# Performance work log

Measured on AMD Instinct MI355X. Metric: run time of the kernel, lower is better.

Reference implementation:

```python
import jax, jax.numpy as jnp
import numpy as np

GRID_SIZE = 5
SPLINE_ORDER = 3
GRID_RANGE = (-1.0, 1.0)
LAYERS = [1024, 1024, 1024]
BATCH = 8192
LN_EPS = 1e-5


def _make_grid(in_features):
    h = (GRID_RANGE[1] - GRID_RANGE[0]) / GRID_SIZE
    n = GRID_SIZE + 2 * SPLINE_ORDER + 1  # 12 knots
    g = jnp.linspace(GRID_RANGE[0] - h * SPLINE_ORDER,
                     GRID_RANGE[1] + h * SPLINE_ORDER, n, dtype=jnp.float32)
    return jnp.broadcast_to(g, (in_features, n))


def setup_inputs() -> dict:
    key = jax.random.key(0)
    ks = jax.random.split(key, 8)
    n_layers = len(LAYERS) - 1
    d_in, d_out = LAYERS[0], LAYERS[1]  # square layers -> stackable params
    coeff = GRID_SIZE + SPLINE_ORDER  # 8
    # kaiming_uniform_(nonlinearity='linear'): bound = sqrt(3) * (1/sqrt(fan_in))
    bw_bound = float(np.sqrt(3.0) / np.sqrt(d_in))
    sw_bound = float(np.sqrt(3.0) / np.sqrt(d_in * coeff))
    x = jax.random.normal(ks[0], (BATCH, d_in), dtype=jnp.float32)
    base_w = jax.random.uniform(ks[1], (n_layers, d_out, d_in), jnp.float32, -bw_bound, bw_bound)
    spline_w = jax.random.uniform(ks[2], (n_layers, d_out, d_in, coeff), jnp.float32, -sw_bound, sw_bound)
    ln_g = jnp.ones((n_layers, d_out), jnp.float32)
    ln_b = jnp.zeros((n_layers, d_out), jnp.float32)
    prelu_a = jnp.full((n_layers,), 0.25, jnp.float32)
    grid = jnp.stack([_make_grid(d_in) for _ in range(n_layers)])  # [L, in, 12]
    return {"x": x, "base_w": base_w, "spline_w": spline_w,
            "ln_g": ln_g, "ln_b": ln_b, "prelu_a": prelu_a, "grid": grid}


def _bspline_bases(x, g):
    """Cox-de Boor recursion. x: [B, in], g: [in, n_knots] -> [B, in, G+order]."""
    xu = x[..., None]  # [B, in, 1]
    bases = ((xu >= g[:, :-1]) & (xu < g[:, 1:])).astype(x.dtype)  # [B, in, 11]
    for k in range(1, SPLINE_ORDER + 1):
        left = g[:, :-(k + 1)]
        right = g[:, k:-1]
        delta = jnp.where(right == left, jnp.ones_like(right), right - left)
        bases = ((xu - left) / delta * bases[..., :-1]
                 + (g[:, k + 1:] - xu) / (g[:, k + 1:] - g[:, 1:-k]) * bases[..., 1:])
    return bases  # [B, in, 8]


def kan_forward(x, base_w, spline_w, ln_g, ln_b, prelu_a, grid):
    n_layers = base_w.shape[0]
    for i in range(n_layers):
        base_out = jnp.matmul(jax.nn.gelu(x, approximate=False), base_w[i].T)  # [B, out]
        bases = _bspline_bases(x, grid[i])  # [B, in, 8]
        spline_out = jnp.matmul(bases.reshape(x.shape[0], -1),
                                spline_w[i].reshape(spline_w.shape[1], -1).T)  # [B, out]
        h = base_out + spline_out
        mu = jnp.mean(h, axis=-1, keepdims=True)
        var = jnp.var(h, axis=-1, keepdims=True)  # biased, matches torch LayerNorm
        h = (h - mu) * jax.lax.rsqrt(var + LN_EPS) * ln_g[i] + ln_b[i]
        x = jnp.where(h >= 0, h, prelu_a[i] * h)  # PReLU (scalar slope per layer)
    return x


def reference(x, base_w, spline_w, ln_g, ln_b, prelu_a, grid):
    return kan_forward(x, base_w, spline_w, ln_g, ln_b, prelu_a, grid)
```

## Files before the change

### kernel.cpp

```cpp
#include <hip/hip_runtime.h>
#include <hip/hip_bf16.h>
#include <cstdint>
#include <cstddef>

typedef __bf16 bf16_t;
typedef __bf16 bf16x8 __attribute__((ext_vector_type(8)));
typedef __bf16 bf16x4 __attribute__((ext_vector_type(4)));
typedef float  f32x4  __attribute__((ext_vector_type(4)));

#define DIM    1024
#define NCOEF  8
#define KTOT   (DIM + DIM * NCOEF)
#define NKNOT  12
#define BATCH  8192
#define LN_EPS 1e-5f

__device__ __forceinline__ float gelu_exact(float x) {
    return 0.5f * x * (1.0f + erff(x * 0.70710678118654752440f));
}

__device__ __forceinline__ void gl_lds16(const void* g, void* l) {
    __builtin_amdgcn_global_load_lds(
        (const __attribute__((address_space(1))) unsigned int*)(uintptr_t)g,
        (__attribute__((address_space(3))) unsigned int*)(uintptr_t)l, 16, 0, 0);
}

__device__ __forceinline__ uint64_t pack4bf(float a, float b, float c, float d) {
    union { bf16_t h[4]; uint64_t q; } u;
    u.h[0] = (bf16_t)a; u.h[1] = (bf16_t)b; u.h[2] = (bf16_t)c; u.h[3] = (bf16_t)d;
    return u.q;
}

__device__ __forceinline__ void spline8(float x, float g0, float invh,
                                        uint64_t& lo, uint64_t& hi) {
    float u = (x - g0) * invh;
    float jf = floorf(u);
    int j = (int)jf;
    float f = u - jf;
    float f2 = f * f, f3 = f2 * f;
    float om = 1.0f - f, om2 = om * om;
    float w0 = om2 * om * (1.0f / 6.0f);
    float w3 = f3 * (1.0f / 6.0f);
    float w1 = fmaf(0.5f, f3, 2.0f / 3.0f) - f2;
    float w2 = 1.0f - w0 - w1 - w3;
    uint64_t W64 = pack4bf(w0, w1, w2, w3);
    if (!(u >= 0.0f && u < 11.0f)) W64 = 0;
    int sh = (j - 3) * 16;
    if (sh >= 0) {
        int s = sh & 63;
        uint64_t loW = W64 << s;
        uint64_t hiW = s ? (W64 >> (64 - s)) : 0ull;
        lo = (sh < 64) ? loW : 0ull;
        hi = (sh < 64) ? hiW : loW;
    } else {
        lo = W64 >> (-sh);
        hi = 0ull;
    }
}

__global__ void pack_w(const float* __restrict__ bw, const float* __restrict__ sw,
                       bf16_t* __restrict__ W) {
    int idx = blockIdx.x * 256 + threadIdx.x;
    bf16_t* wrow = W + (size_t)(idx >> 10) * KTOT;
    int j = idx & 1023;
    wrow[j] = (bf16_t)bw[idx];
    const float4* sp = (const float4*)(sw + (size_t)idx * NCOEF);
    float4 s0 = sp[0], s1 = sp[1];
    bf16x8 v;
    v[0] = (bf16_t)s0.x; v[1] = (bf16_t)s0.y; v[2] = (bf16_t)s0.z; v[3] = (bf16_t)s0.w;
    v[4] = (bf16_t)s1.x; v[5] = (bf16_t)s1.y; v[6] = (bf16_t)s1.z; v[7] = (bf16_t)s1.w;
    *(bf16x8*)(wrow + DIM + j * NCOEF) = v;
}

__global__ void prep_A(const float* __restrict__ x, bf16_t* __restrict__ A,
                       const float* __restrict__ gp) {
    const int row = blockIdx.x, t = threadIdx.x;
    const float g0 = gp[0];
    const float invh = 1.0f / (gp[1] - gp[0]);
    f32x4 v = *(const f32x4*)(x + (size_t)row * DIM + t * 4);
    bf16_t* Ar = A + (size_t)row * KTOT;
    bf16x4 ge;
#pragma unroll
    for (int k = 0; k < 4; k++) ge[k] = (bf16_t)gelu_exact(v[k]);
    *(bf16x4*)(Ar + t * 4) = ge;
#pragma unroll
    for (int k = 0; k < 4; k++) {
        uint64_t lo, hi;
        union { uint64_t u[2]; uint4 q; } o;
        spline8(v[k], g0, invh, lo, hi);
        o.u[0] = lo; o.u[1] = hi;
        *(uint4*)(Ar + DIM + (t * 4 + k) * NCOEF) = o.q;
    }
}


#define STR2(x) #x
#define GATEV(N) asm volatile("s_waitcnt vmcnt(" STR2(N) ")" ::: "memory");
#define LGKM(N)  asm volatile("s_waitcnt lgkmcnt(" STR2(N) ")" ::: "memory");
#define BAR() { __builtin_amdgcn_s_barrier(); asm volatile("" ::: "memory"); }

#define MF_ROW(I, A_) \
    acc[I][0] = __builtin_amdgcn_mfma_f32_16x16x32_bf16(A_, b0, acc[I][0], 0, 0, 0); \
    acc[I][1] = __builtin_amdgcn_mfma_f32_16x16x32_bf16(A_, b1, acc[I][1], 0, 0, 0); \
    acc[I][2] = __builtin_amdgcn_mfma_f32_16x16x32_bf16(A_, b2, acc[I][2], 0, 0, 0); \
    acc[I][3] = __builtin_amdgcn_mfma_f32_16x16x32_bf16(A_, b3, acc[I][3], 0, 0, 0);

#define TILE(T, S, SN, SP, DOSTAGE, GATESTMT, DOEARLY, WAITB) { \
     \
    if (DOSTAGE) { \
      gl_lds16(Ag0 + (size_t)((T) + 3) * 32, ldsA + (SP) * 8192 + tid * 8); \
      gl_lds16(Ag1 + (size_t)((T) + 3) * 32, ldsA + (SP) * 8192 + 4096 + tid * 8); } \
    BAR() \
    { const bf16_t* Ab_ = ldsA + (S) * 8192 + aOff; \
      a4 = *(const bf16x8*)(Ab_ + 2048); a5 = *(const bf16x8*)(Ab_ + 2560); \
      a6 = *(const bf16x8*)(Ab_ + 3072); a7 = *(const bf16x8*)(Ab_ + 3584); } \
    LGKM(4) \
    __builtin_amdgcn_sched_barrier(0); \
    __builtin_amdgcn_s_setprio(1); \
    MF_ROW(0, a0) MF_ROW(1, a1) MF_ROW(2, a2) MF_ROW(3, a3) \
    __builtin_amdgcn_s_setprio(0); \
    BAR() \
     \
    if (DOSTAGE) { \
      gl_lds16(Bg0 + (size_t)((T) + 3) * 32, ldsB + (SP) * 8192 + tid * 8); \
      gl_lds16(Bg1 + (size_t)((T) + 3) * 32, ldsB + (SP) * 8192 + 4096 + tid * 8); } \
    GATESTMT \
    BAR() \
    if (DOEARLY) { \
      const bf16_t* An_ = ldsA + (SN) * 8192 + aOff; \
      const bf16_t* Bn_ = ldsB + (SN) * 8192 + bOff; \
      na0 = *(const bf16x8*)(An_);        na1 = *(const bf16x8*)(An_ + 512); \
      na2 = *(const bf16x8*)(An_ + 1024); na3 = *(const bf16x8*)(An_ + 1536); \
      nb0 = *(const bf16x8*)(Bn_);        nb1 = *(const bf16x8*)(Bn_ + 512); \
      nb2 = *(const bf16x8*)(Bn_ + 1024); nb3 = *(const bf16x8*)(Bn_ + 1536); } \
    WAITB \
    __builtin_amdgcn_sched_barrier(0); \
    __builtin_amdgcn_s_setprio(1); \
    MF_ROW(4, a4) MF_ROW(5, a5) MF_ROW(6, a6) MF_ROW(7, a7) \
    __builtin_amdgcn_s_setprio(0); \
    BAR() \
    a0 = na0; a1 = na1; a2 = na2; a3 = na3; \
    b0 = nb0; b1 = nb1; b2 = nb2; b3 = nb3; \
}

#define PSTAGE(T, S) \
    gl_lds16(Ag0 + (size_t)(T) * 32, ldsA + (S) * 8192 + tid * 8); \
    gl_lds16(Ag1 + (size_t)(T) * 32, ldsA + (S) * 8192 + 4096 + tid * 8); \
    gl_lds16(Bg0 + (size_t)(T) * 32, ldsB + (S) * 8192 + tid * 8); \
    gl_lds16(Bg1 + (size_t)(T) * 32, ldsB + (S) * 8192 + 4096 + tid * 8);

template<int NTK>
__global__ __launch_bounds__(512, 2) void gemm_ab(
    const bf16_t* __restrict__ A,
    const bf16_t* __restrict__ W,
    float* __restrict__ C,
    int mmask, int mshift, int rows) {
    __shared__ __align__(16) bf16_t lds[65536];
    bf16_t* __restrict__ ldsA = lds;
    bf16_t* __restrict__ ldsB = lds + 32768;

    const int tid = threadIdx.x;
    const int l = tid & 63, wv = tid >> 6;
    const int wm = wv >> 2, wn = wv & 3;

    const int chunk = gridDim.x >> 3;
    const int bid = blockIdx.x;
    const int wg = (bid & 7) * chunk + (bid >> 3);
    const int bm = wg & mmask;
    const int bn = (wg >> mshift) & 3;
    const int ks = wg >> (mshift + 2);
    const int row0 = bm << 8, col0 = bn << 8;
    const int koff0 = ks * (NTK * 32);

    const int srow = tid >> 2;
    const int slc = (tid & 3) ^ ((srow >> 1) & 3);
    const bf16_t* __restrict__ Ag0 = A + (size_t)(row0 + srow) * KTOT + koff0 + slc * 8;
    const bf16_t* __restrict__ Ag1 = Ag0 + (size_t)128 * KTOT;
    const bf16_t* __restrict__ Bg0 = W + (size_t)(col0 + srow) * KTOT + koff0 + slc * 8;
    const bf16_t* __restrict__ Bg1 = Bg0 + (size_t)128 * KTOT;

    const int l15 = l & 15;
    const int pc = (l >> 4) ^ ((l15 >> 1) & 3);
    const int aOff = (wm * 128 + l15) * 32 + pc * 8;
    const int bOff = (wn * 64 + l15) * 32 + pc * 8;

    f32x4 acc[8][4] = {};
    bf16x8 a0, a1, a2, a3, a4, a5, a6, a7, b0, b1, b2, b3;
    bf16x8 na0, na1, na2, na3, nb0, nb1, nb2, nb3;

    PSTAGE(0, 0)
    PSTAGE(1, 1)
    PSTAGE(2, 2)
    GATEV(8)
    BAR()
    {
        const bf16_t* An_ = ldsA + aOff;
        const bf16_t* Bn_ = ldsB + bOff;
        a0 = *(const bf16x8*)(An_);        a1 = *(const bf16x8*)(An_ + 512);
        a2 = *(const bf16x8*)(An_ + 1024); a3 = *(const bf16x8*)(An_ + 1536);
        b0 = *(const bf16x8*)(Bn_);        b1 = *(const bf16x8*)(Bn_ + 512);
        b2 = *(const bf16x8*)(Bn_ + 1024); b3 = *(const bf16x8*)(Bn_ + 1536);
    }

#pragma unroll 1
    for (int t = 0; t < NTK - 4; t += 4) {
        TILE(t + 0, 0, 1, 3, 1, GATEV(8), 1, LGKM(8))
        TILE(t + 1, 1, 2, 0, 1, GATEV(8), 1, LGKM(8))
        TILE(t + 2, 2, 3, 1, 1, GATEV(8), 1, LGKM(8))
        TILE(t + 3, 3, 0, 2, 1, GATEV(8), 1, LGKM(8))
    }
    TILE(NTK - 4, 0, 1, 3, 1, GATEV(8), 1, LGKM(8))
    TILE(NTK - 3, 1, 2, 0, 0, GATEV(4), 1, LGKM(8))
    TILE(NTK - 2, 2, 3, 1, 0, GATEV(0), 1, LGKM(8))
    TILE(NTK - 1, 3, 0, 2, 0, ;,        0, LGKM(0))

    float* __restrict__ Cp = C + (size_t)ks * rows * DIM;
    const int r0 = row0 + wm * 128 + (l >> 4) * 4;
    const int c0 = col0 + wn * 64 + l15;
#pragma unroll
    for (int i = 0; i < 8; i++)
#pragma unroll
        for (int j = 0; j < 4; j++)
#pragma unroll
            for (int r = 0; r < 4; r++)
                Cp[(size_t)(r0 + i * 16 + r) * DIM + c0 + j * 16] = acc[i][j][r];
}

__global__ void ln_mid_A(const float* __restrict__ h, int rows, int ksplit,
                         const float* __restrict__ g_ln, const float* __restrict__ b_ln,
                         const float* __restrict__ pa, bf16_t* __restrict__ A,
                         const float* __restrict__ gp) {
    const int row = blockIdx.x, tid = threadIdx.x;
    const int w = tid >> 6, l = tid & 63;
    f32x4 v = {0.0f, 0.0f, 0.0f, 0.0f};
    for (int ks = 0; ks < ksplit; ks++)
        v += *(const f32x4*)(h + ((size_t)ks * rows + row) * DIM + tid * 4);
    float s = v[0] + v[1] + v[2] + v[3];
    float q = v[0] * v[0] + v[1] * v[1] + v[2] * v[2] + v[3] * v[3];
#pragma unroll
    for (int o = 32; o > 0; o >>= 1) { s += __shfl_xor(s, o); q += __shfl_xor(q, o); }
    __shared__ float rs[4], rq[4];
    if (l == 0) { rs[w] = s; rq[w] = q; }
    __syncthreads();
    s = rs[0] + rs[1] + rs[2] + rs[3];
    q = rq[0] + rq[1] + rq[2] + rq[3];
    float mean = s * (1.0f / DIM);
    float var = q * (1.0f / DIM) - mean * mean;
    float rstd = rsqrtf(var + LN_EPS);
    float a = pa[0];
    const float g0 = gp[0];
    const float invh = 1.0f / (gp[1] - gp[0]);
    bf16_t* Ar = A + (size_t)row * KTOT;
    bf16x4 ge;
#pragma unroll
    for (int c = 0; c < 4; c++) {
        int col = tid * 4 + c;
        float yv = (v[c] - mean) * rstd * g_ln[col] + b_ln[col];
        yv = (yv >= 0.0f) ? yv : a * yv;
        ge[c] = (bf16_t)gelu_exact(yv);
        uint64_t lo, hi;
        union { uint64_t u[2]; uint4 qv; } o;
        spline8(yv, g0, invh, lo, hi);
        o.u[0] = lo; o.u[1] = hi;
        *(uint4*)(Ar + DIM + (size_t)col * NCOEF) = o.qv;
    }
    *(bf16x4*)(Ar + tid * 4) = ge;
}

__global__ void ln_out(const float* __restrict__ h, int rows, int ksplit,
                       const float* __restrict__ g_ln, const float* __restrict__ b_ln,
                       const float* __restrict__ pa, float* __restrict__ out) {
    const int row = blockIdx.x, tid = threadIdx.x;
    const int w = tid >> 6, l = tid & 63;
    f32x4 v = {0.0f, 0.0f, 0.0f, 0.0f};
    for (int ks = 0; ks < ksplit; ks++)
        v += *(const f32x4*)(h + ((size_t)ks * rows + row) * DIM + tid * 4);
    float s = v[0] + v[1] + v[2] + v[3];
    float q = v[0] * v[0] + v[1] * v[1] + v[2] * v[2] + v[3] * v[3];
#pragma unroll
    for (int o = 32; o > 0; o >>= 1) { s += __shfl_xor(s, o); q += __shfl_xor(q, o); }
    __shared__ float rs[4], rq[4];
    if (l == 0) { rs[w] = s; rq[w] = q; }
    __syncthreads();
    s = rs[0] + rs[1] + rs[2] + rs[3];
    q = rq[0] + rq[1] + rq[2] + rq[3];
    float mean = s * (1.0f / DIM);
    float var = q * (1.0f / DIM) - mean * mean;
    float rstd = rsqrtf(var + LN_EPS);
    float a = pa[0];
    f32x4 o4;
#pragma unroll
    for (int c = 0; c < 4; c++) {
        int col = tid * 4 + c;
        float yv = (v[c] - mean) * rstd * g_ln[col] + b_ln[col];
        o4[c] = (yv >= 0.0f) ? yv : a * yv;
    }
    *(f32x4*)(out + (size_t)row * DIM + tid * 4) = o4;
}

extern "C" void kernel_launch(void* const* d_in, const int* in_sizes, int n_in,
                              void* d_out, int out_size, void* d_ws, size_t ws_size,
                              hipStream_t stream) {
    const float* x    = (const float*)d_in[0];
    const float* bw   = (const float*)d_in[1];
    const float* sw   = (const float*)d_in[2];
    const float* ln_g = (const float*)d_in[3];
    const float* ln_b = (const float*)d_in[4];
    const float* pa   = (const float*)d_in[5];
    const float* gridK = (const float*)d_in[6];
    float* out = (float*)d_out;

    const size_t wbytes = (size_t)2 * DIM * KTOT * sizeof(bf16_t);
    int R = 8192, ksplit = 2;
    for (;;) {
        size_t need = wbytes + (size_t)R * KTOT * 2 + (size_t)ksplit * R * DIM * 4;
        if (need <= ws_size || R == 512) break;
        R >>= 1;
        int mt = R / 256;
        ksplit = (mt >= 32) ? 2 : (mt >= 16) ? 4 : 8;
    }
    int mtiles = R / 256;
    int mshift = 0; while ((1 << mshift) < mtiles) mshift++;
    int mmask = mtiles - 1;
    int grid = mtiles * 4 * ksplit;

    char* wsc = (char*)d_ws;
    bf16_t* Wbuf = (bf16_t*)wsc;
    bf16_t* Abuf = (bf16_t*)(wsc + wbytes);
    float*  hbuf = (float*)(wsc + wbytes + (size_t)R * KTOT * 2);

    pack_w<<<(2 * DIM * DIM) / 256, 256, 0, stream>>>(bw, sw, Wbuf);

    auto launch_gemm = [&](const bf16_t* Wl, hipStream_t st) {
        if (ksplit == 2)
            gemm_ab<144><<<grid, 512, 0, st>>>(Abuf, Wl, hbuf, mmask, mshift, R);
        else if (ksplit == 4)
            gemm_ab<72><<<grid, 512, 0, st>>>(Abuf, Wl, hbuf, mmask, mshift, R);
        else
            gemm_ab<36><<<grid, 512, 0, st>>>(Abuf, Wl, hbuf, mmask, mshift, R);
    };

    const int nslab = BATCH / R;
    for (int sidx = 0; sidx < nslab; sidx++) {
        const size_t row0 = (size_t)sidx * R;
        const float* x0 = x + row0 * DIM;
        prep_A<<<R, 256, 0, stream>>>(x0, Abuf, gridK);
        launch_gemm(Wbuf, stream);
        ln_mid_A<<<R, 256, 0, stream>>>(hbuf, R, ksplit, ln_g, ln_b, pa,
                                        Abuf, gridK + DIM * NKNOT);
        launch_gemm(Wbuf + (size_t)DIM * KTOT, stream);
        ln_out<<<R, 256, 0, stream>>>(hbuf, R, ksplit, ln_g + DIM, ln_b + DIM,
                                      pa + 1, out + row0 * DIM);
    }
}
```

Before: 568.2 us.

## Double-buffer GEMM fragment registers to drop barriers; grid-stride elementwise kernels

The GEMM main loop now alternates between two named register sets (even/odd) for A/B fragments instead of copying next-tile fragments into current registers. This removes the register copies and two of the four block barriers per K-tile, leaving one barrier before the early LDS reads and one at tile end. The prep, mid-layernorm and output-layernorm kernels become grid-stride loops over a capped grid of 2048 blocks, which cuts block launch overhead. Fewer barriers could expose LDS write-after-read hazards across the 4-stage ring, and the extra fragment registers raise VGPR pressure under the 2-waves-per-SIMD launch bound.

```diff
diff --git a/kernel.cpp b/kernel.cpp
--- a/kernel.cpp
+++ b/kernel.cpp
@@ -73,23 +73,25 @@
 }
 
 __global__ void prep_A(const float* __restrict__ x, bf16_t* __restrict__ A,
-                       const float* __restrict__ gp) {
-    const int row = blockIdx.x, t = threadIdx.x;
+                       const float* __restrict__ gp, int R) {
+    const int t = threadIdx.x;
     const float g0 = gp[0];
     const float invh = 1.0f / (gp[1] - gp[0]);
-    f32x4 v = *(const f32x4*)(x + (size_t)row * DIM + t * 4);
-    bf16_t* Ar = A + (size_t)row * KTOT;
-    bf16x4 ge;
-#pragma unroll
-    for (int k = 0; k < 4; k++) ge[k] = (bf16_t)gelu_exact(v[k]);
-    *(bf16x4*)(Ar + t * 4) = ge;
-#pragma unroll
-    for (int k = 0; k < 4; k++) {
-        uint64_t lo, hi;
-        union { uint64_t u[2]; uint4 q; } o;
-        spline8(v[k], g0, invh, lo, hi);
-        o.u[0] = lo; o.u[1] = hi;
-        *(uint4*)(Ar + DIM + (t * 4 + k) * NCOEF) = o.q;
+    for (int row = blockIdx.x; row < R; row += gridDim.x) {
+        f32x4 v = *(const f32x4*)(x + (size_t)row * DIM + t * 4);
+        bf16_t* Ar = A + (size_t)row * KTOT;
+        bf16x4 ge;
+#pragma unroll
+        for (int k = 0; k < 4; k++) ge[k] = (bf16_t)gelu_exact(v[k]);
+        *(bf16x4*)(Ar + t * 4) = ge;
+#pragma unroll
+        for (int k = 0; k < 4; k++) {
+            uint64_t lo, hi;
+            union { uint64_t u[2]; uint4 q; } o;
+            spline8(v[k], g0, invh, lo, hi);
+            o.u[0] = lo; o.u[1] = hi;
+            *(uint4*)(Ar + DIM + (t * 4 + k) * NCOEF) = o.q;
+        }
     }
 }
 
@@ -99,48 +101,51 @@
 #define LGKM(N)  asm volatile("s_waitcnt lgkmcnt(" STR2(N) ")" ::: "memory");
 #define BAR() { __builtin_amdgcn_s_barrier(); asm volatile("" ::: "memory"); }
 
-#define MF_ROW(I, A_) \
-    acc[I][0] = __builtin_amdgcn_mfma_f32_16x16x32_bf16(A_, b0, acc[I][0], 0, 0, 0); \
-    acc[I][1] = __builtin_amdgcn_mfma_f32_16x16x32_bf16(A_, b1, acc[I][1], 0, 0, 0); \
-    acc[I][2] = __builtin_amdgcn_mfma_f32_16x16x32_bf16(A_, b2, acc[I][2], 0, 0, 0); \
-    acc[I][3] = __builtin_amdgcn_mfma_f32_16x16x32_bf16(A_, b3, acc[I][3], 0, 0, 0);
-
-#define TILE(T, S, SN, SP, DOSTAGE, GATESTMT, DOEARLY, WAITB) { \
+#define EA(i) ea##i
+#define EB(i) eb##i
+#define OA(i) oa##i
+#define OB(i) ob##i
+
+#define MF_ROWX(I, A_, CB) \
+    acc[I][0] = __builtin_amdgcn_mfma_f32_16x16x32_bf16(A_, CB(0), acc[I][0], 0, 0, 0); \
+    acc[I][1] = __builtin_amdgcn_mfma_f32_16x16x32_bf16(A_, CB(1), acc[I][1], 0, 0, 0); \
+    acc[I][2] = __builtin_amdgcn_mfma_f32_16x16x32_bf16(A_, CB(2), acc[I][2], 0, 0, 0); \
+    acc[I][3] = __builtin_amdgcn_mfma_f32_16x16x32_bf16(A_, CB(3), acc[I][3], 0, 0, 0);
+
+#define TILE(T, S, SN, SP, STG, GATESTMT, RD, WAITB, CA, CB, NA, NB) { \
      \
-    if (DOSTAGE) { \
+    if (STG) { \
       gl_lds16(Ag0 + (size_t)((T) + 3) * 32, ldsA + (SP) * 8192 + tid * 8); \
       gl_lds16(Ag1 + (size_t)((T) + 3) * 32, ldsA + (SP) * 8192 + 4096 + tid * 8); } \
-    BAR() \
     { const bf16_t* Ab_ = ldsA + (S) * 8192 + aOff; \
-      a4 = *(const bf16x8*)(Ab_ + 2048); a5 = *(const bf16x8*)(Ab_ + 2560); \
-      a6 = *(const bf16x8*)(Ab_ + 3072); a7 = *(const bf16x8*)(Ab_ + 3584); } \
+      CA(4) = *(const bf16x8*)(Ab_ + 2048); CA(5) = *(const bf16x8*)(Ab_ + 2560); \
+      CA(6) = *(const bf16x8*)(Ab_ + 3072); CA(7) = *(const bf16x8*)(Ab_ + 3584); } \
     LGKM(4) \
     __builtin_amdgcn_sched_barrier(0); \
     __builtin_amdgcn_s_setprio(1); \
-    MF_ROW(0, a0) MF_ROW(1, a1) MF_ROW(2, a2) MF_ROW(3, a3) \
+    MF_ROWX(0, CA(0), CB) MF_ROWX(1, CA(1), CB) \
+    MF_ROWX(2, CA(2), CB) MF_ROWX(3, CA(3), CB) \
     __builtin_amdgcn_s_setprio(0); \
-    BAR() \
      \
-    if (DOSTAGE) { \
+    if (STG) { \
       gl_lds16(Bg0 + (size_t)((T) + 3) * 32, ldsB + (SP) * 8192 + tid * 8); \
       gl_lds16(Bg1 + (size_t)((T) + 3) * 32, ldsB + (SP) * 8192 + 4096 + tid * 8); } \
     GATESTMT \
-    BAR() \
-    if (DOEARLY) { \
+    if (RD) { \
+      BAR() \
       const bf16_t* An_ = ldsA + (SN) * 8192 + aOff; \
       const bf16_t* Bn_ = ldsB + (SN) * 8192 + bOff; \
-      na0 = *(const bf16x8*)(An_);        na1 = *(const bf16x8*)(An_ + 512); \
-      na2 = *(const bf16x8*)(An_ + 1024); na3 = *(const bf16x8*)(An_ + 1536); \
-      nb0 = *(const bf16x8*)(Bn_);        nb1 = *(const bf16x8*)(Bn_ + 512); \
-      nb2 = *(const bf16x8*)(Bn_ + 1024); nb3 = *(const bf16x8*)(Bn_ + 1536); } \
+      NA(0) = *(const bf16x8*)(An_);        NA(1) = *(const bf16x8*)(An_ + 512); \
+      NA(2) = *(const bf16x8*)(An_ + 1024); NA(3) = *(const bf16x8*)(An_ + 1536); \
+      NB(0) = *(const bf16x8*)(Bn_);        NB(1) = *(const bf16x8*)(Bn_ + 512); \
+      NB(2) = *(const bf16x8*)(Bn_ + 1024); NB(3) = *(const bf16x8*)(Bn_ + 1536); } \
     WAITB \
     __builtin_amdgcn_sched_barrier(0); \
     __builtin_amdgcn_s_setprio(1); \
-    MF_ROW(4, a4) MF_ROW(5, a5) MF_ROW(6, a6) MF_ROW(7, a7) \
+    MF_ROWX(4, CA(4), CB) MF_ROWX(5, CA(5), CB) \
+    MF_ROWX(6, CA(6), CB) MF_ROWX(7, CA(7), CB) \
     __builtin_amdgcn_s_setprio(0); \
     BAR() \
-    a0 = na0; a1 = na1; a2 = na2; a3 = na3; \
-    b0 = nb0; b1 = nb1; b2 = nb2; b3 = nb3; \
 }
 
 #define PSTAGE(T, S) \
@@ -185,8 +190,8 @@
     const int bOff = (wn * 64 + l15) * 32 + pc * 8;
 
     f32x4 acc[8][4] = {};
-    bf16x8 a0, a1, a2, a3, a4, a5, a6, a7, b0, b1, b2, b3;
-    bf16x8 na0, na1, na2, na3, nb0, nb1, nb2, nb3;
+    bf16x8 ea0, ea1, ea2, ea3, ea4, ea5, ea6, ea7, eb0, eb1, eb2, eb3;
+    bf16x8 oa0, oa1, oa2, oa3, oa4, oa5, oa6, oa7, ob0, ob1, ob2, ob3;
 
     PSTAGE(0, 0)
     PSTAGE(1, 1)
@@ -196,23 +201,23 @@
     {
         const bf16_t* An_ = ldsA + aOff;
         const bf16_t* Bn_ = ldsB + bOff;
-        a0 = *(const bf16x8*)(An_);        a1 = *(const bf16x8*)(An_ + 512);
-        a2 = *(const bf16x8*)(An_ + 1024); a3 = *(const bf16x8*)(An_ + 1536);
-        b0 = *(const bf16x8*)(Bn_);        b1 = *(const bf16x8*)(Bn_ + 512);
-        b2 = *(const bf16x8*)(Bn_ + 1024); b3 = *(const bf16x8*)(Bn_ + 1536);
+        ea0 = *(const bf16x8*)(An_);        ea1 = *(const bf16x8*)(An_ + 512);
+        ea2 = *(const bf16x8*)(An_ + 1024); ea3 = *(const bf16x8*)(An_ + 1536);
+        eb0 = *(const bf16x8*)(Bn_);        eb1 = *(const bf16x8*)(Bn_ + 512);
+        eb2 = *(const bf16x8*)(Bn_ + 1024); eb3 = *(const bf16x8*)(Bn_ + 1536);
     }
 
 #pragma unroll 1
     for (int t = 0; t < NTK - 4; t += 4) {
-        TILE(t + 0, 0, 1, 3, 1, GATEV(8), 1, LGKM(8))
-        TILE(t + 1, 1, 2, 0, 1, GATEV(8), 1, LGKM(8))
-        TILE(t + 2, 2, 3, 1, 1, GATEV(8), 1, LGKM(8))
-        TILE(t + 3, 3, 0, 2, 1, GATEV(8), 1, LGKM(8))
-    }
-    TILE(NTK - 4, 0, 1, 3, 1, GATEV(8), 1, LGKM(8))
-    TILE(NTK - 3, 1, 2, 0, 0, GATEV(4), 1, LGKM(8))
-    TILE(NTK - 2, 2, 3, 1, 0, GATEV(0), 1, LGKM(8))
-    TILE(NTK - 1, 3, 0, 2, 0, ;,        0, LGKM(0))
+        TILE(t + 0, 0, 1, 3, 1, GATEV(8), 1, LGKM(8), EA, EB, OA, OB)
+        TILE(t + 1, 1, 2, 0, 1, GATEV(8), 1, LGKM(8), OA, OB, EA, EB)
+        TILE(t + 2, 2, 3, 1, 1, GATEV(8), 1, LGKM(8), EA, EB, OA, OB)
+        TILE(t + 3, 3, 0, 2, 1, GATEV(8), 1, LGKM(8), OA, OB, EA, EB)
+    }
+    TILE(NTK - 4, 0, 1, 3, 1, GATEV(8), 1, LGKM(8), EA, EB, OA, OB)
+    TILE(NTK - 3, 1, 2, 0, 0, GATEV(4), 1, LGKM(8), OA, OB, EA, EB)
+    TILE(NTK - 2, 2, 3, 1, 0, GATEV(0), 1, LGKM(8), EA, EB, OA, OB)
+    TILE(NTK - 1, 3, 0, 2, 0, GATEV(0), 0, LGKM(0), OA, OB, EA, EB)
 
     float* __restrict__ Cp = C + (size_t)ks * rows * DIM;
     const int r0 = row0 + wm * 128 + (l >> 4) * 4;
@@ -230,72 +235,78 @@
                          const float* __restrict__ g_ln, const float* __restrict__ b_ln,
                          const float* __restrict__ pa, bf16_t* __restrict__ A,
                          const float* __restrict__ gp) {
-    const int row = blockIdx.x, tid = threadIdx.x;
+    const int tid = threadIdx.x;
     const int w = tid >> 6, l = tid & 63;
-    f32x4 v = {0.0f, 0.0f, 0.0f, 0.0f};
-    for (int ks = 0; ks < ksplit; ks++)
-        v += *(const f32x4*)(h + ((size_t)ks * rows + row) * DIM + tid * 4);
-    float s = v[0] + v[1] + v[2] + v[3];
-    float q = v[0] * v[0] + v[1] * v[1] + v[2] * v[2] + v[3] * v[3];
-#pragma unroll
-    for (int o = 32; o > 0; o >>= 1) { s += __shfl_xor(s, o); q += __shfl_xor(q, o); }
-    __shared__ float rs[4], rq[4];
-    if (l == 0) { rs[w] = s; rq[w] = q; }
-    __syncthreads();
-    s = rs[0] + rs[1] + rs[2] + rs[3];
-    q = rq[0] + rq[1] + rq[2] + rq[3];
-    float mean = s * (1.0f / DIM);
-    float var = q * (1.0f / DIM) - mean * mean;
-    float rstd = rsqrtf(var + LN_EPS);
-    float a = pa[0];
+    const float a = pa[0];
     const float g0 = gp[0];
     const float invh = 1.0f / (gp[1] - gp[0]);
-    bf16_t* Ar = A + (size_t)row * KTOT;
-    bf16x4 ge;
-#pragma unroll
-    for (int c = 0; c < 4; c++) {
-        int col = tid * 4 + c;
-        float yv = (v[c] - mean) * rstd * g_ln[col] + b_ln[col];
-        yv = (yv >= 0.0f) ? yv : a * yv;
-        ge[c] = (bf16_t)gelu_exact(yv);
-        uint64_t lo, hi;
-        union { uint64_t u[2]; uint4 qv; } o;
-        spline8(yv, g0, invh, lo, hi);
-        o.u[0] = lo; o.u[1] = hi;
-        *(uint4*)(Ar + DIM + (size_t)col * NCOEF) = o.qv;
-    }
-    *(bf16x4*)(Ar + tid * 4) = ge;
+    __shared__ float rs[4], rq[4];
+    for (int row = blockIdx.x; row < rows; row += gridDim.x) {
+        f32x4 v = {0.0f, 0.0f, 0.0f, 0.0f};
+        for (int ks = 0; ks < ksplit; ks++)
+            v += *(const f32x4*)(h + ((size_t)ks * rows + row) * DIM + tid * 4);
+        float s = v[0] + v[1] + v[2] + v[3];
+        float q = v[0] * v[0] + v[1] * v[1] + v[2] * v[2] + v[3] * v[3];
+#pragma unroll
+        for (int o = 32; o > 0; o >>= 1) { s += __shfl_xor(s, o); q += __shfl_xor(q, o); }
+        if (l == 0) { rs[w] = s; rq[w] = q; }
+        __syncthreads();
+        s = rs[0] + rs[1] + rs[2] + rs[3];
+        q = rq[0] + rq[1] + rq[2] + rq[3];
+        __syncthreads();
+        float mean = s * (1.0f / DIM);
+        float var = q * (1.0f / DIM) - mean * mean;
+        float rstd = rsqrtf(var + LN_EPS);
+        bf16_t* Ar = A + (size_t)row * KTOT;
+        bf16x4 ge;
+#pragma unroll
+        for (int c = 0; c < 4; c++) {
+            int col = tid * 4 + c;
+            float yv = (v[c] - mean) * rstd * g_ln[col] + b_ln[col];
+            yv = (yv >= 0.0f) ? yv : a * yv;
+            ge[c] = (bf16_t)gelu_exact(yv);
+            uint64_t lo, hi;
+            union { uint64_t u[2]; uint4 qv; } o;
+            spline8(yv, g0, invh, lo, hi);
+            o.u[0] = lo; o.u[1] = hi;
+            *(uint4*)(Ar + DIM + (size_t)col * NCOEF) = o.qv;
+        }
+        *(bf16x4*)(Ar + tid * 4) = ge;
+    }
 }
 
 __global__ void ln_out(const float* __restrict__ h, int rows, int ksplit,
                        const float* __restrict__ g_ln, const float* __restrict__ b_ln,
                        const float* __restrict__ pa, float* __restrict__ out) {
-    const int row = blockIdx.x, tid = threadIdx.x;
+    const int tid = threadIdx.x;
     const int w = tid >> 6, l = tid & 63;
-    f32x4 v = {0.0f, 0.0f, 0.0f, 0.0f};
-    for (int ks = 0; ks < ksplit; ks++)
-        v += *(const f32x4*)(h + ((size_t)ks * rows + row) * DIM + tid * 4);
-    float s = v[0] + v[1] + v[2] + v[3];
-    float q = v[0] * v[0] + v[1] * v[1] + v[2] * v[2] + v[3] * v[3];
-#pragma unroll
-    for (int o = 32; o > 0; o >>= 1) { s += __shfl_xor(s, o); q += __shfl_xor(q, o); }
+    const float a = pa[0];
     __shared__ float rs[4], rq[4];
-    if (l == 0) { rs[w] = s; rq[w] = q; }
-    __syncthreads();
-    s = rs[0] + rs[1] + rs[2] + rs[3];
-    q = rq[0] + rq[1] + rq[2] + rq[3];
-    float mean = s * (1.0f / DIM);
-    float var = q * (1.0f / DIM) - mean * mean;
-    float rstd = rsqrtf(var + LN_EPS);
-    float a = pa[0];
-    f32x4 o4;
-#pragma unroll
-    for (int c = 0; c < 4; c++) {
-        int col = tid * 4 + c;
-        float yv = (v[c] - mean) * rstd * g_ln[col] + b_ln[col];
-        o4[c] = (yv >= 0.0f) ? yv : a * yv;
-    }
-    *(f32x4*)(out + (size_t)row * DIM + tid * 4) = o4;
+    for (int row = blockIdx.x; row < rows; row += gridDim.x) {
+        f32x4 v = {0.0f, 0.0f, 0.0f, 0.0f};
+        for (int ks = 0; ks < ksplit; ks++)
+            v += *(const f32x4*)(h + ((size_t)ks * rows + row) * DIM + tid * 4);
+        float s = v[0] + v[1] + v[2] + v[3];
+        float q = v[0] * v[0] + v[1] * v[1] + v[2] * v[2] + v[3] * v[3];
+#pragma unroll
+        for (int o = 32; o > 0; o >>= 1) { s += __shfl_xor(s, o); q += __shfl_xor(q, o); }
+        if (l == 0) { rs[w] = s; rq[w] = q; }
+        __syncthreads();
+        s = rs[0] + rs[1] + rs[2] + rs[3];
+        q = rq[0] + rq[1] + rq[2] + rq[3];
+        __syncthreads();
+        float mean = s * (1.0f / DIM);
+        float var = q * (1.0f / DIM) - mean * mean;
+        float rstd = rsqrtf(var + LN_EPS);
+        f32x4 o4;
+#pragma unroll
+        for (int c = 0; c < 4; c++) {
+            int col = tid * 4 + c;
+            float yv = (v[c] - mean) * rstd * g_ln[col] + b_ln[col];
+            o4[c] = (yv >= 0.0f) ? yv : a * yv;
+        }
+        *(f32x4*)(out + (size_t)row * DIM + tid * 4) = o4;
+    }
 }
 
 extern "C" void kernel_launch(void* const* d_in, const int* in_sizes, int n_in,
@@ -323,6 +334,7 @@
     int mshift = 0; while ((1 << mshift) < mtiles) mshift++;
     int mmask = mtiles - 1;
     int grid = mtiles * 4 * ksplit;
+    int lng = (R >= 2048) ? 2048 : R;
 
     char* wsc = (char*)d_ws;
     bf16_t* Wbuf = (bf16_t*)wsc;
@@ -344,12 +356,12 @@
     for (int sidx = 0; sidx < nslab; sidx++) {
         const size_t row0 = (size_t)sidx * R;
         const float* x0 = x + row0 * DIM;
-        prep_A<<<R, 256, 0, stream>>>(x0, Abuf, gridK);
+        prep_A<<<lng, 256, 0, stream>>>(x0, Abuf, gridK, R);
         launch_gemm(Wbuf, stream);
-        ln_mid_A<<<R, 256, 0, stream>>>(hbuf, R, ksplit, ln_g, ln_b, pa,
-                                        Abuf, gridK + DIM * NKNOT);
+        ln_mid_A<<<lng, 256, 0, stream>>>(hbuf, R, ksplit, ln_g, ln_b, pa,
+                                          Abuf, gridK + DIM * NKNOT);
         launch_gemm(Wbuf + (size_t)DIM * KTOT, stream);
-        ln_out<<<R, 256, 0, stream>>>(hbuf, R, ksplit, ln_g + DIM, ln_b + DIM,
-                                      pa + 1, out + row0 * DIM);
-    }
-}
+        ln_out<<<lng, 256, 0, stream>>>(hbuf, R, ksplit, ln_g + DIM, ln_b + DIM,
+                                        pa + 1, out + row0 * DIM);
+    }
+}
```

Result: no change. 574.8 us (+1.2%).
